# Kernel tuning notes

Hardware: AMD Instinct MI355X
Metric: run time of the kernel (lower is better)

Reference implementation:

```python
import jax, jax.numpy as jnp
import numpy as np

CHANNEL = 1
ALPHA = 1.0
EPS = 1e-10
SHAPE = (1, CHANNEL, 160, 192, 160)


def _sobel_kernels(channel):
    s2 = np.array([[-1., 0., 1.], [-2., 0., 2.], [-1., 0., 1.]], dtype=np.float32)
    # sobel.repeat(channel,1,3,1,1): 2D kernel tiled along depth -> k[d,h,w] = s2[h,w]
    kx = np.tile(s2[None, :, :], (3, 1, 1))
    ky = np.tile(s2.T[None, :, :], (3, 1, 1))
    kz = np.array([[[-1., -1., -1.], [-2., -2., -2.], [-1., -1., -1.]],
                   [[0., 0., 0.], [0., 0., 0.], [0., 0., 0.]],
                   [[1., 1., 1.], [2., 2., 2.], [1., 1., 1.]]], dtype=np.float32)
    def rep(k):  # -> [channel, 1, 3, 3, 3] for depthwise conv
        return jnp.asarray(np.tile(k[None, None], (channel, 1, 1, 1, 1)))
    return rep(kx), rep(ky), rep(kz)


def _conv3d(x, k, channel):
    # torch F.conv3d (cross-correlation), padding=1, groups=channel
    return jax.lax.conv_general_dilated(
        x, k, window_strides=(1, 1, 1), padding=((1, 1), (1, 1), (1, 1)),
        dimension_numbers=('NCDHW', 'OIDHW', 'NCDHW'),
        feature_group_count=channel)


def setup_inputs() -> dict:
    key = jax.random.key(0)
    k1, k2, k3 = jax.random.split(key, 3)
    M = jax.random.normal(k1, SHAPE, dtype=jnp.float32)
    S = jax.random.normal(k2, SHAPE, dtype=jnp.float32)
    flow = jax.random.normal(k3, (SHAPE[0], 3) + SHAPE[2:], dtype=jnp.float32)
    return {"M": M, "S": S, "flow": flow}


def reference(M, S, flow):
    kx, ky, kz = _sobel_kernels(CHANNEL)
    Idiff = M - S
    Sx = _conv3d(S, kx, CHANNEL)
    Sy = _conv3d(S, ky, CHANNEL)
    Sz = _conv3d(S, kz, CHANNEL)
    Mx = _conv3d(M, kx, CHANNEL)
    My = _conv3d(M, ky, CHANNEL)
    Mz = _conv3d(M, kz, CHANNEL)
    Sxyz_mag = Sx ** 2 + Sy ** 2 + Sz ** 2
    Mxyz_mag = Mx ** 2 + My ** 2 + Mz ** 2
    denom_S = Sxyz_mag + (ALPHA ** 2) * Idiff ** 2 + 1e-10
    denom_M = Mxyz_mag + (ALPHA ** 2) * Idiff ** 2 + 1e-10
    Ux = Idiff * (Sx / denom_S + Mx / denom_M)
    Uy = Idiff * (Sy / denom_S + My / denom_M)
    Uz = Idiff * (Sz / denom_S + Mz / denom_M)
    demons_ori_xz = jnp.arctan(Ux / (Uz + EPS))
    demons_ori_yz = jnp.arctan(Uy / (Uz + EPS))
    flow_ori_xz = jnp.arctan(flow[:, 0] / (flow[:, 2] + EPS))
    flow_ori_yz = jnp.arctan(flow[:, 1] / (flow[:, 2] + EPS))
    ori_error = jnp.mean((flow_ori_xz - demons_ori_xz) ** 2) + \
                jnp.mean((flow_ori_yz - demons_ori_yz) ** 2)
    return ori_error
```

## Files before the change

### kernel.cpp

```cpp
#include <hip/hip_runtime.h>
#include <math.h>

#define DD 160
#define HH 192
#define WW 160
#define TW 32
#define THB 16
#define TD 8
#define HW (HH * WW)
#define NVOX (DD * HW)
#define WROWS 4
#define WHR 6
#define WHW 34
#define WHALO (WHR * WHW)
#define WSTR 208

typedef float v2f __attribute__((ext_vector_type(2)));

__device__ __forceinline__ v2f vrcp(v2f a) {
    v2f r;
    r.x = __builtin_amdgcn_rcpf(a.x);
    r.y = __builtin_amdgcn_rcpf(a.y);
    return r;
}

__device__ __forceinline__ v2f atan_ratio(v2f num, v2f den) {
    v2f a = __builtin_elementwise_abs(num);
    v2f b = __builtin_elementwise_abs(den);
    v2f mn = __builtin_elementwise_min(a, b);
    v2f mx = __builtin_elementwise_max(a, b);
    v2f x = mn * vrcp(mx);
    v2f x2 = x * x;
    v2f p = __builtin_elementwise_fma(x2,
            __builtin_elementwise_fma(x2,
            __builtin_elementwise_fma(x2,
            __builtin_elementwise_fma(x2,
            __builtin_elementwise_fma(x2, (v2f)(-0.0117212f), (v2f)(0.05265332f)),
            (v2f)(-0.11643287f)), (v2f)(0.19354346f)), (v2f)(-0.33262347f)),
            (v2f)(0.99997726f));
    p *= x;
    v2f q = 1.57079632679489662f - p;
    v2f res;
    res.x = a.x > b.x ? q.x : p.x;
    res.y = a.y > b.y ? q.y : p.y;
    unsigned sx = (__float_as_uint(num.x) ^ __float_as_uint(den.x)) & 0x80000000u;
    unsigned sy = (__float_as_uint(num.y) ^ __float_as_uint(den.y)) & 0x80000000u;
    res.x = __uint_as_float(__float_as_uint(res.x) | sx);
    res.y = __uint_as_float(__float_as_uint(res.y) | sy);
    return res;
}

struct Part { v2f Px, Py, B, C; };

__global__ __launch_bounds__(256) void demons_ori_kernel(
    const float* __restrict__ Mv, const float* __restrict__ Sv,
    const float* __restrict__ flow, float* __restrict__ out)
{
    __shared__ float buf[4][2][2][WSTR];
    __shared__ float redbuf[4];

    const int tid = threadIdx.x;
    const int lane = tid & 63;
    const int wid = tid >> 6;
    const int i16 = lane & 15;
    const int rloc = lane >> 4;
    const int tw2 = 2 * i16;
    const int w0 = blockIdx.x * TW;
    const int hbase = blockIdx.y * THB + wid * WROWS;
    const int gh = hbase + rloc;
    const int d0 = blockIdx.z * TD;

    const bool has3 = (lane < WHALO - 192);
    int gb[4]; bool ok[4];
    #pragma unroll
    for (int s = 0; s < 4; ++s) {
        int i = lane + 64 * s;
        int hh = i / WHW, ww = i - WHW * hh;
        int ghs = hbase + hh - 1, gws = w0 + ww - 1;
        bool act = (s < 3) || has3;
        ok[s] = act && (ghs >= 0) && (ghs < HH) && (gws >= 0) && (gws < WW);
        gb[s] = ghs * WW + gws;
    }

    float hS[4], hM[4];

    auto issue = [&](int d) {
        const bool din = ((unsigned)d < (unsigned)DD);
        const size_t base = (size_t)d * HW;
        #pragma unroll
        for (int s = 0; s < 4; ++s) {
            bool o = din && ok[s];
            hS[s] = o ? Sv[base + gb[s]] : 0.f;
            hM[s] = o ? Mv[base + gb[s]] : 0.f;
        }
    };
    auto commit = [&](int d) {
        float* __restrict__ bS = &buf[wid][d & 1][0][0];
        float* __restrict__ bM = &buf[wid][d & 1][1][0];
        #pragma unroll
        for (int s = 0; s < 3; ++s) {
            bS[lane + 64 * s] = hS[s];
            bM[lane + 64 * s] = hM[s];
        }
        if (has3) { bS[lane + 192] = hS[3]; bM[lane + 192] = hM[3]; }
    };

    const int rb = rloc * WHW + tw2;
    auto fieldPartials = [&](const float* __restrict__ b, Part& P) {
        const float* p0 = b + rb;
        const float* p1 = p0 + WHW;
        const float* p2 = p1 + WHW;
        v2f lo0 = *(const v2f*)p0, hi0 = *(const v2f*)(p0 + 2);
        v2f lo1 = *(const v2f*)p1, hi1 = *(const v2f*)(p1 + 2);
        v2f lo2 = *(const v2f*)p2, hi2 = *(const v2f*)(p2 + 2);
        v2f X0 = hi0 - lo0, X1 = hi1 - lo1, X2 = hi2 - lo2;
        v2f m0 = (v2f){lo0.y, hi0.x};
        v2f m1 = (v2f){lo1.y, hi1.x};
        v2f m2 = (v2f){lo2.y, hi2.x};
        v2f s0 = lo0 + hi0, s1 = lo1 + hi1, s2 = lo2 + hi2;
        v2f W0 = __builtin_elementwise_fma(m0, (v2f)(2.f), s0);
        v2f W2 = __builtin_elementwise_fma(m2, (v2f)(2.f), s2);
        v2f I0 = s0 + m0, I1 = s1 + m1, I2 = s2 + m2;
        P.Px = __builtin_elementwise_fma(X1, (v2f)(2.f), X0) + X2;
        P.Py = W2 - W0;
        P.B  = __builtin_elementwise_fma(I1, (v2f)(2.f), I0) + I2;
        P.C  = m1;
    };

    Part mS, zS, pS, mM, zM, pM;

    issue(d0 - 1);
    commit(d0 - 1);
    issue(d0);
    fieldPartials(&buf[wid][(d0 - 1) & 1][0][0], mS);
    fieldPartials(&buf[wid][(d0 - 1) & 1][1][0], mM);
    commit(d0);
    issue(d0 + 1);
    fieldPartials(&buf[wid][d0 & 1][0][0], zS);
    fieldPartials(&buf[wid][d0 & 1][1][0], zM);

    const size_t voff = (size_t)gh * WW + (w0 + tw2);
    v2f fFx, fFy, fFz;
    {
        size_t o = (size_t)d0 * HW + voff;
        fFx = *(const v2f*)(flow + o);
        fFy = *(const v2f*)(flow + NVOX + o);
        fFz = *(const v2f*)(flow + 2 * (size_t)NVOX + o);
    }

    v2f vsum = (v2f){0.f, 0.f};

    #pragma unroll
    for (int dd = 0; dd < TD; ++dd) {
        const int d = d0 + dd;
        commit(d + 1);
        v2f nFx = (v2f){0.f, 0.f}, nFy = nFx, nFz = nFx;
        if (dd < TD - 1) {
            issue(d + 2);
            size_t o = (size_t)(d + 1) * HW + voff;
            nFx = *(const v2f*)(flow + o);
            nFy = *(const v2f*)(flow + NVOX + o);
            nFz = *(const v2f*)(flow + 2 * (size_t)NVOX + o);
        }
        fieldPartials(&buf[wid][(d + 1) & 1][0][0], pS);
        fieldPartials(&buf[wid][(d + 1) & 1][1][0], pM);

        v2f idf = zM.C - zS.C;
        v2f i2  = __builtin_elementwise_fma(idf, idf, (v2f)(1e-10f));
        v2f gxS = mS.Px + zS.Px + pS.Px;
        v2f gyS = mS.Py + zS.Py + pS.Py;
        v2f gzS = pS.B - mS.B;
        v2f gxM = mM.Px + zM.Px + pM.Px;
        v2f gyM = mM.Py + zM.Py + pM.Py;
        v2f gzM = pM.B - mM.B;
        v2f denS = __builtin_elementwise_fma(gxS, gxS,
                   __builtin_elementwise_fma(gyS, gyS,
                   __builtin_elementwise_fma(gzS, gzS, i2)));
        v2f denM = __builtin_elementwise_fma(gxM, gxM,
                   __builtin_elementwise_fma(gyM, gyM,
                   __builtin_elementwise_fma(gzM, gzM, i2)));
        v2f rS = vrcp(denS);
        v2f rM = vrcp(denM);
        v2f Ux = idf * __builtin_elementwise_fma(gxS, rS, gxM * rM);
        v2f Uy = idf * __builtin_elementwise_fma(gyS, rS, gyM * rM);
        v2f Uz = idf * __builtin_elementwise_fma(gzS, rS, gzM * rM);

        v2f uzp = Uz + 1e-10f;
        v2f dxz = atan_ratio(Ux, uzp);
        v2f dyz = atan_ratio(Uy, uzp);

        v2f fzp = fFz + 1e-10f;
        v2f fxz = atan_ratio(fFx, fzp);
        v2f fyz = atan_ratio(fFy, fzp);

        v2f e1 = fxz - dxz;
        v2f e2 = fyz - dyz;
        vsum = __builtin_elementwise_fma(e1, e1,
               __builtin_elementwise_fma(e2, e2, vsum));

        mS = zS; zS = pS;
        mM = zM; zM = pM;
        fFx = nFx; fFy = nFy; fFz = nFz;
    }

    float lsum = vsum.x + vsum.y;
    #pragma unroll
    for (int o = 32; o > 0; o >>= 1)
        lsum += __shfl_down(lsum, o, 64);
    if (lane == 0)
        redbuf[wid] = lsum;
    __syncthreads();
    if (tid == 0) {
        float s = redbuf[0] + redbuf[1] + redbuf[2] + redbuf[3];
        atomicAdd(out, s * (1.0f / (float)NVOX));
    }
}

extern "C" void kernel_launch(void* const* d_in, const int* in_sizes, int n_in,
                              void* d_out, int out_size, void* d_ws, size_t ws_size,
                              hipStream_t stream) {
    const float* Mv   = (const float*)d_in[0];
    const float* Sv   = (const float*)d_in[1];
    const float* flow = (const float*)d_in[2];
    float* out = (float*)d_out;

    hipMemsetAsync(out, 0, sizeof(float), stream);

    dim3 grid(WW / TW, HH / THB, DD / TD);
    demons_ori_kernel<<<grid, dim3(256), 0, stream>>>(Mv, Sv, flow, out);
}
```

Baseline: 156.7 us.

## Share block-wide halo tile and process two depth slices per step

Replaces the per-wave private 6x34 halo buffers with one block-wide 18x34 halo tile shared by all four waves, synchronized with __syncthreads. This cuts the redundant reloads of halo rows between neighbouring waves. Each iteration now loads and consumes two depth slices at once, double-buffered in shared memory, and prefetches flow for both slices. The cost is block-level barriers and more registers held for in-flight loads and flow values, which may reduce occupancy.

```diff
diff --git a/kernel.cpp b/kernel.cpp
--- a/kernel.cpp
+++ b/kernel.cpp
@@ -9,11 +9,11 @@
 #define TD 8
 #define HW (HH * WW)
 #define NVOX (DD * HW)
-#define WROWS 4
-#define WHR 6
-#define WHW 34
-#define WHALO (WHR * WHW)
-#define WSTR 208
+#define HTW 34
+#define HTH 18
+#define LSTR 34
+#define PHALO 612
+#define PAIRH 1224
 
 typedef float v2f __attribute__((ext_vector_type(2)));
 
@@ -56,60 +56,80 @@
     const float* __restrict__ Mv, const float* __restrict__ Sv,
     const float* __restrict__ flow, float* __restrict__ out)
 {
-    __shared__ float buf[4][2][2][WSTR];
+    __shared__ float buf[2][2][PAIRH];
     __shared__ float redbuf[4];
 
     const int tid = threadIdx.x;
     const int lane = tid & 63;
     const int wid = tid >> 6;
     const int i16 = lane & 15;
-    const int rloc = lane >> 4;
+    const int r   = wid * 4 + (lane >> 4);
     const int tw2 = 2 * i16;
     const int w0 = blockIdx.x * TW;
-    const int hbase = blockIdx.y * THB + wid * WROWS;
-    const int gh = hbase + rloc;
+    const int h0 = blockIdx.y * THB;
     const int d0 = blockIdx.z * TD;
 
-    const bool has3 = (lane < WHALO - 192);
-    int gb[4]; bool ok[4];
-    #pragma unroll
-    for (int s = 0; s < 4; ++s) {
-        int i = lane + 64 * s;
-        int hh = i / WHW, ww = i - WHW * hh;
-        int ghs = hbase + hh - 1, gws = w0 + ww - 1;
-        bool act = (s < 3) || has3;
-        ok[s] = act && (ghs >= 0) && (ghs < HH) && (gws >= 0) && (gws < WW);
-        gb[s] = ghs * WW + gws;
-    }
-
-    float hS[4], hM[4];
-
-    auto issue = [&](int d) {
-        const bool din = ((unsigned)d < (unsigned)DD);
-        const size_t base = (size_t)d * HW;
-        #pragma unroll
-        for (int s = 0; s < 4; ++s) {
-            bool o = din && ok[s];
-            hS[s] = o ? Sv[base + gb[s]] : 0.f;
-            hM[s] = o ? Mv[base + gb[s]] : 0.f;
+    const bool has4 = (tid < PAIRH - 1024);
+    int gb0, gb1, gb2, gb3, gb4 = 0;
+    int pl0, pl1, pl2, pl3, pl4 = 0;
+    bool ok0, ok1, ok2, ok3, ok4 = false;
+    {
+        int i, j, hh, ww, gh, gw;
+        i = tid;           pl0 = 0;            j = i;
+        hh = j / HTW; ww = j - HTW * hh; gh = h0 + hh - 1; gw = w0 + ww - 1;
+        ok0 = (gh >= 0 && gh < HH && gw >= 0 && gw < WW); gb0 = gh * WW + gw;
+        i = tid + 256;     pl1 = (i >= PHALO); j = i - PHALO * pl1;
+        hh = j / HTW; ww = j - HTW * hh; gh = h0 + hh - 1; gw = w0 + ww - 1;
+        ok1 = (gh >= 0 && gh < HH && gw >= 0 && gw < WW); gb1 = gh * WW + gw;
+        i = tid + 512;     pl2 = (i >= PHALO); j = i - PHALO * pl2;
+        hh = j / HTW; ww = j - HTW * hh; gh = h0 + hh - 1; gw = w0 + ww - 1;
+        ok2 = (gh >= 0 && gh < HH && gw >= 0 && gw < WW); gb2 = gh * WW + gw;
+        i = tid + 768;     pl3 = 1;            j = i - PHALO;
+        hh = j / HTW; ww = j - HTW * hh; gh = h0 + hh - 1; gw = w0 + ww - 1;
+        ok3 = (gh >= 0 && gh < HH && gw >= 0 && gw < WW); gb3 = gh * WW + gw;
+        if (has4) {
+            i = tid + 1024; pl4 = 1;           j = i - PHALO;
+            hh = j / HTW; ww = j - HTW * hh; gh = h0 + hh - 1; gw = w0 + ww - 1;
+            ok4 = (gh >= 0 && gh < HH && gw >= 0 && gw < WW); gb4 = gh * WW + gw;
         }
-    };
-    auto commit = [&](int d) {
-        float* __restrict__ bS = &buf[wid][d & 1][0][0];
-        float* __restrict__ bM = &buf[wid][d & 1][1][0];
-        #pragma unroll
-        for (int s = 0; s < 3; ++s) {
-            bS[lane + 64 * s] = hS[s];
-            bM[lane + 64 * s] = hM[s];
-        }
-        if (has3) { bS[lane + 192] = hS[3]; bM[lane + 192] = hM[3]; }
-    };
-
-    const int rb = rloc * WHW + tw2;
+    }
+
+    float hS0 = 0.f, hM0 = 0.f, hS1 = 0.f, hM1 = 0.f, hS2 = 0.f, hM2 = 0.f;
+    float hS3 = 0.f, hM3 = 0.f, hS4 = 0.f, hM4 = 0.f;
+
+    auto issue = [&](int e) {
+        int dp; bool o; size_t a;
+        dp = e + pl0; o = ok0 && ((unsigned)dp < (unsigned)DD);
+        a = (size_t)dp * HW + gb0;
+        hS0 = o ? Sv[a] : 0.f;  hM0 = o ? Mv[a] : 0.f;
+        dp = e + pl1; o = ok1 && ((unsigned)dp < (unsigned)DD);
+        a = (size_t)dp * HW + gb1;
+        hS1 = o ? Sv[a] : 0.f;  hM1 = o ? Mv[a] : 0.f;
+        dp = e + pl2; o = ok2 && ((unsigned)dp < (unsigned)DD);
+        a = (size_t)dp * HW + gb2;
+        hS2 = o ? Sv[a] : 0.f;  hM2 = o ? Mv[a] : 0.f;
+        dp = e + pl3; o = ok3 && ((unsigned)dp < (unsigned)DD);
+        a = (size_t)dp * HW + gb3;
+        hS3 = o ? Sv[a] : 0.f;  hM3 = o ? Mv[a] : 0.f;
+        dp = e + pl4; o = ok4 && ((unsigned)dp < (unsigned)DD);
+        a = (size_t)dp * HW + gb4;
+        hS4 = o ? Sv[a] : 0.f;  hM4 = o ? Mv[a] : 0.f;
+    };
+    auto commit = [&](int par) {
+        float* __restrict__ bS = &buf[par][0][0];
+        float* __restrict__ bM = &buf[par][1][0];
+        bS[tid] = hS0;         bM[tid] = hM0;
+        bS[tid + 256] = hS1;   bM[tid + 256] = hM1;
+        bS[tid + 512] = hS2;   bM[tid + 512] = hM2;
+        bS[tid + 768] = hS3;   bM[tid + 768] = hM3;
+        if (has4) { bS[tid + 1024] = hS4; bM[tid + 1024] = hM4; }
+    };
+
+    const int rb = r * LSTR + tw2;
     auto fieldPartials = [&](const float* __restrict__ b, Part& P) {
         const float* p0 = b + rb;
-        const float* p1 = p0 + WHW;
-        const float* p2 = p1 + WHW;
+        const float* p1 = p0 + LSTR;
+        const float* p2 = p1 + LSTR;
         v2f lo0 = *(const v2f*)p0, hi0 = *(const v2f*)(p0 + 2);
         v2f lo1 = *(const v2f*)p1, hi1 = *(const v2f*)(p1 + 2);
         v2f lo2 = *(const v2f*)p2, hi2 = *(const v2f*)(p2 + 2);
@@ -127,44 +147,11 @@
         P.C  = m1;
     };
 
-    Part mS, zS, pS, mM, zM, pM;
-
-    issue(d0 - 1);
-    commit(d0 - 1);
-    issue(d0);
-    fieldPartials(&buf[wid][(d0 - 1) & 1][0][0], mS);
-    fieldPartials(&buf[wid][(d0 - 1) & 1][1][0], mM);
-    commit(d0);
-    issue(d0 + 1);
-    fieldPartials(&buf[wid][d0 & 1][0][0], zS);
-    fieldPartials(&buf[wid][d0 & 1][1][0], zM);
-
-    const size_t voff = (size_t)gh * WW + (w0 + tw2);
-    v2f fFx, fFy, fFz;
-    {
-        size_t o = (size_t)d0 * HW + voff;
-        fFx = *(const v2f*)(flow + o);
-        fFy = *(const v2f*)(flow + NVOX + o);
-        fFz = *(const v2f*)(flow + 2 * (size_t)NVOX + o);
-    }
-
     v2f vsum = (v2f){0.f, 0.f};
 
-    #pragma unroll
-    for (int dd = 0; dd < TD; ++dd) {
-        const int d = d0 + dd;
-        commit(d + 1);
-        v2f nFx = (v2f){0.f, 0.f}, nFy = nFx, nFz = nFx;
-        if (dd < TD - 1) {
-            issue(d + 2);
-            size_t o = (size_t)(d + 1) * HW + voff;
-            nFx = *(const v2f*)(flow + o);
-            nFy = *(const v2f*)(flow + NVOX + o);
-            nFz = *(const v2f*)(flow + 2 * (size_t)NVOX + o);
-        }
-        fieldPartials(&buf[wid][(d + 1) & 1][0][0], pS);
-        fieldPartials(&buf[wid][(d + 1) & 1][1][0], pM);
-
+    auto sliceTerm = [&](const Part& mS, const Part& zS, const Part& pS,
+                         const Part& mM, const Part& zM, const Part& pM,
+                         v2f fx, v2f fy, v2f fz) {
         v2f idf = zM.C - zS.C;
         v2f i2  = __builtin_elementwise_fma(idf, idf, (v2f)(1e-10f));
         v2f gxS = mS.Px + zS.Px + pS.Px;
@@ -184,23 +171,72 @@
         v2f Ux = idf * __builtin_elementwise_fma(gxS, rS, gxM * rM);
         v2f Uy = idf * __builtin_elementwise_fma(gyS, rS, gyM * rM);
         v2f Uz = idf * __builtin_elementwise_fma(gzS, rS, gzM * rM);
-
         v2f uzp = Uz + 1e-10f;
         v2f dxz = atan_ratio(Ux, uzp);
         v2f dyz = atan_ratio(Uy, uzp);
-
-        v2f fzp = fFz + 1e-10f;
-        v2f fxz = atan_ratio(fFx, fzp);
-        v2f fyz = atan_ratio(fFy, fzp);
-
+        v2f fzp = fz + 1e-10f;
+        v2f fxz = atan_ratio(fx, fzp);
+        v2f fyz = atan_ratio(fy, fzp);
         v2f e1 = fxz - dxz;
         v2f e2 = fyz - dyz;
         vsum = __builtin_elementwise_fma(e1, e1,
                __builtin_elementwise_fma(e2, e2, vsum));
-
-        mS = zS; zS = pS;
-        mM = zM; zM = pM;
-        fFx = nFx; fFy = nFy; fFz = nFz;
+    };
+
+    Part mS, zS, pS, qS, mM, zM, pM, qM;
+
+    issue(d0 - 1);
+    commit(1);
+    issue(d0 + 1);
+    __syncthreads();
+    fieldPartials(&buf[1][0][0], mS);
+    fieldPartials(&buf[1][1][0], mM);
+    fieldPartials(&buf[1][0][PHALO], zS);
+    fieldPartials(&buf[1][1][PHALO], zM);
+
+    const size_t voff = (size_t)(h0 + r) * WW + (w0 + tw2);
+    v2f fAx, fAy, fAz, fBx, fBy, fBz;
+    {
+        size_t o = (size_t)d0 * HW + voff;
+        fAx = *(const v2f*)(flow + o);
+        fAy = *(const v2f*)(flow + NVOX + o);
+        fAz = *(const v2f*)(flow + 2 * (size_t)NVOX + o);
+        o += HW;
+        fBx = *(const v2f*)(flow + o);
+        fBy = *(const v2f*)(flow + NVOX + o);
+        fBz = *(const v2f*)(flow + 2 * (size_t)NVOX + o);
+    }
+
+    #pragma unroll
+    for (int k = 0; k < TD / 2; ++k) {
+        const int d = d0 + 2 * k;
+        const int par = k & 1;
+        commit(par);
+        v2f nAx = (v2f){0.f, 0.f}, nAy = nAx, nAz = nAx;
+        v2f nBx = nAx, nBy = nAx, nBz = nAx;
+        if (k < TD / 2 - 1) {
+            issue(d + 3);
+            size_t o = (size_t)(d + 2) * HW + voff;
+            nAx = *(const v2f*)(flow + o);
+            nAy = *(const v2f*)(flow + NVOX + o);
+            nAz = *(const v2f*)(flow + 2 * (size_t)NVOX + o);
+            o += HW;
+            nBx = *(const v2f*)(flow + o);
+            nBy = *(const v2f*)(flow + NVOX + o);
+            nBz = *(const v2f*)(flow + 2 * (size_t)NVOX + o);
+        }
+        __syncthreads();
+        fieldPartials(&buf[par][0][0], pS);
+        fieldPartials(&buf[par][1][0], pM);
+        sliceTerm(mS, zS, pS, mM, zM, pM, fAx, fAy, fAz);
+        fieldPartials(&buf[par][0][PHALO], qS);
+        fieldPartials(&buf[par][1][PHALO], qM);
+        sliceTerm(zS, pS, qS, zM, pM, qM, fBx, fBy, fBz);
+
+        mS = pS; zS = qS;
+        mM = pM; zM = qM;
+        fAx = nAx; fAy = nAy; fAz = nAz;
+        fBx = nBx; fBy = nBy; fBz = nBz;
     }
 
     float lsum = vsum.x + vsum.y;
```

New measurement: 129.5 us. 1.21x faster.
